# Optimization experiments

Measured on AMD Instinct MI355X. Metric: run time of the kernel, lower is better.

The kernel has to match this reference:

```python
import jax, jax.numpy as jnp
import numpy as np

INPUTS_SIZE = 128
HIDDEN_SIZE = 256
BATCH = 65536


def hard_sigmoid(x):
    # torch.nn.Hardsigmoid: relu6(x + 3) / 6
    return jnp.clip(x / 6.0 + 0.5, 0.0, 1.0)


def hard_tanh(x):
    return jnp.clip(x, -1.0, 1.0)


def setup_inputs() -> dict:
    key = jax.random.key(0)
    ks = jax.random.split(key, 8)
    cat = INPUTS_SIZE + HIDDEN_SIZE
    s = 1.0 / np.sqrt(cat)
    return {
        "inputs": jax.random.normal(ks[0], (BATCH, INPUTS_SIZE), dtype=jnp.float32),
        "h_prev": jax.random.normal(ks[1], (BATCH, HIDDEN_SIZE), dtype=jnp.float32),
        "W_z": jax.random.uniform(ks[2], (HIDDEN_SIZE, cat), jnp.float32, -s, s),
        "b_z": jax.random.uniform(ks[3], (HIDDEN_SIZE,), jnp.float32, -s, s),
        "W_r": jax.random.uniform(ks[4], (HIDDEN_SIZE, cat), jnp.float32, -s, s),
        "b_r": jax.random.uniform(ks[5], (HIDDEN_SIZE,), jnp.float32, -s, s),
        "W_h": jax.random.uniform(ks[6], (HIDDEN_SIZE, cat), jnp.float32, -s, s),
        "b_h": jax.random.uniform(ks[7], (HIDDEN_SIZE,), jnp.float32, -s, s),
    }


def reference(inputs, h_prev, W_z, b_z, W_r, b_r, W_h, b_h):
    # concat(inputs, h_prev) along feature dim: [B, I+H]
    ih = jnp.concatenate([inputs, h_prev], axis=-1)
    # update gate z and reset gate r (HardSigmoid activations)
    z = hard_sigmoid(ih @ W_z.T + b_z)  # [B, H]
    r = hard_sigmoid(ih @ W_r.T + b_r)  # [B, H]
    # candidate: concat(inputs, r * h_prev) -> linear -> HardTanh
    irh = jnp.concatenate([inputs, r * h_prev], axis=-1)
    h_tilde = hard_tanh(irh @ W_h.T + b_h)  # [B, H]
    # h_next = z * h_prev + (1 - z) * h_tilde
    h_next = z * h_prev + (1.0 - z) * h_tilde
    return h_next
```

## Files before the change

### kernel.cpp

```cpp
#include <hip/hip_runtime.h>


#define BATCH   65536
#define ISZ     128
#define HSZ     256
#define CAT     384
#define BM      64
#define NT      512
#define ROWB    768
#define ACT_B   (BM * ROWB)
#define WBUF_B  32768

using half8   = __attribute__((ext_vector_type(8))) _Float16;
using floatx4 = __attribute__((ext_vector_type(4))) float;

#define WAITV asm volatile("s_waitcnt vmcnt(0)" ::: "memory")

typedef unsigned int u32;
typedef __attribute__((address_space(1))) const u32 gu32;
typedef __attribute__((address_space(3))) u32 lu32;

__device__ __forceinline__ void gload16(const void* g, void* l) {
    __builtin_amdgcn_global_load_lds((gu32*)g, (lu32*)l, 16, 0, 0);
}

__device__ __forceinline__ float hsig(float x) {
    return fminf(fmaxf(x * (1.0f / 6.0f) + 0.5f, 0.0f), 1.0f);
}
__device__ __forceinline__ float htanh(float x) {
    return fminf(fmaxf(x, -1.0f), 1.0f);
}
__device__ __forceinline__ half8 cvt8(float4 v0, float4 v1) {
    half8 h;
    h[0] = (_Float16)v0.x; h[1] = (_Float16)v0.y;
    h[2] = (_Float16)v0.z; h[3] = (_Float16)v0.w;
    h[4] = (_Float16)v1.x; h[5] = (_Float16)v1.y;
    h[6] = (_Float16)v1.z; h[7] = (_Float16)v1.w;
    return h;
}

__global__ __launch_bounds__(256) void prep_weights(
    const float* __restrict__ Wz, const float* __restrict__ Wr,
    const float* __restrict__ Wh, _Float16* __restrict__ ws)
{
    const int m = blockIdx.y;
    const float* src = (m == 0) ? Wz : (m == 1) ? Wr : Wh;
    _Float16* dst = ws + (size_t)m * (HSZ * CAT);
    const int base = (blockIdx.x * 256 + threadIdx.x) * 8;
    float4 v0 = *(const float4*)(src + base);
    float4 v1 = *(const float4*)(src + base + 4);
    *(half8*)(dst + base) = cvt8(v0, v1);
}

__device__ __forceinline__ void issue_w(const _Float16* __restrict__ wsrc,
                                        unsigned char* wdst, int w, int lane,
                                        int kk, int nper) {
    #pragma unroll
    for (int ii = 0; ii < nper; ++ii) {
        const int i = w * nper + ii;
        const int n = i * 16 + (lane >> 2);
        const int sslot = (lane & 3) ^ ((n >> 1) & 3);
        gload16(wsrc + n * CAT + kk * 32 + sslot * 8, wdst + i * 1024);
    }
}

__device__ __forceinline__ half8 wread(const unsigned char* wbuf, int n, int lk) {
    return *(const half8*)(wbuf + n * 64 + ((lk ^ ((n >> 1) & 3)) << 4));
}

__global__ __launch_bounds__(NT, 4) void gru_kernel(
    const float* __restrict__ x, const float* __restrict__ h_prev,
    const float* __restrict__ b_z, const float* __restrict__ b_r,
    const float* __restrict__ b_h, const _Float16* __restrict__ wf,
    float* __restrict__ out)
{
    __shared__ __align__(16) unsigned char lds[ACT_B + WBUF_B];
    unsigned char* const act  = lds;
    unsigned char* const wbuf = lds + ACT_B;

    const int t    = threadIdx.x;
    const int lane = t & 63;
    const int w    = t >> 6;
    const int mg   = w >> 2;
    const int ng   = w & 3;
    const int lr   = lane & 15;
    const int lk   = lane >> 4;
    const int row0 = blockIdx.x * BM;
    const _Float16* wh = wf + 2 * HSZ * CAT;

    issue_w(wf, wbuf, w, lane, 0, 4);

    for (int c = t; c < BM * 16; c += NT) {
        int row = c >> 4, kc = c & 15;
        const float* g = x + (size_t)(row0 + row) * ISZ + kc * 8;
        float4 v0 = *(const float4*)g;
        float4 v1 = *(const float4*)(g + 4);
        *(half8*)(act + row * ROWB + ((kc * 16) ^ ((row & 7) << 4))) = cvt8(v0, v1);
    }
    for (int c = t; c < BM * 32; c += NT) {
        int row = c >> 5, kc = c & 31;
        const float* g = h_prev + (size_t)(row0 + row) * HSZ + kc * 8;
        float4 v0 = *(const float4*)g;
        float4 v1 = *(const float4*)(g + 4);
        *(half8*)(act + row * ROWB + ((256 + kc * 16) ^ ((row & 7) << 4))) = cvt8(v0, v1);
    }
    WAITV;
    __syncthreads();

    floatx4 accz[2][4] = {};
    floatx4 accr[2][4] = {};
    const int rowA = mg * 32 + lr;
    const int asw  = (rowA & 7) << 4;

    #pragma unroll 1
    for (int kk = 0; kk < 12; ++kk) {
        half8 a0 = *(const half8*)(act + rowA * ROWB        + ((kk * 64 + lk * 16) ^ asw));
        half8 a1 = *(const half8*)(act + (rowA + 16) * ROWB + ((kk * 64 + lk * 16) ^ asw));
        half8 bf[4];
        #pragma unroll
        for (int j = 0; j < 4; ++j) bf[j] = wread(wbuf, ng * 64 + j * 16 + lr, lk);
        #pragma unroll
        for (int j = 0; j < 4; ++j) {
            accz[0][j] = __builtin_amdgcn_mfma_f32_16x16x32_f16(a0, bf[j], accz[0][j], 0, 0, 0);
            accz[1][j] = __builtin_amdgcn_mfma_f32_16x16x32_f16(a1, bf[j], accz[1][j], 0, 0, 0);
        }
        #pragma unroll
        for (int j = 0; j < 4; ++j) bf[j] = wread(wbuf, 256 + ng * 64 + j * 16 + lr, lk);
        #pragma unroll
        for (int j = 0; j < 4; ++j) {
            accr[0][j] = __builtin_amdgcn_mfma_f32_16x16x32_f16(a0, bf[j], accr[0][j], 0, 0, 0);
            accr[1][j] = __builtin_amdgcn_mfma_f32_16x16x32_f16(a1, bf[j], accr[1][j], 0, 0, 0);
        }
        __syncthreads();
        if (kk < 11) {
            issue_w(wf, wbuf, w, lane, kk + 1, 4);
            WAITV;
            __syncthreads();
        }
    }

    issue_w(wh, wbuf, w, lane, 0, 2);

    float bzv[4], brv[4];
    #pragma unroll
    for (int j = 0; j < 4; ++j) {
        int col = ng * 64 + j * 16 + lr;
        bzv[j] = b_z[col];
        brv[j] = b_r[col];
    }
    #pragma unroll
    for (int f = 0; f < 2; ++f) {
        #pragma unroll
        for (int j = 0; j < 4; ++j) {
            #pragma unroll
            for (int q = 0; q < 4; ++q) {
                int row = mg * 32 + f * 16 + lk * 4 + q;
                int col = ng * 64 + j * 16 + lr;
                accz[f][j][q] = hsig(accz[f][j][q] + bzv[j]);
                float rr = hsig(accr[f][j][q] + brv[j]);
                _Float16* hp = (_Float16*)(act + row * ROWB +
                                           ((256 + col * 2) ^ ((row & 7) << 4)));
                float hv = (float)hp[0];
                hp[0] = (_Float16)(rr * hv);
            }
        }
    }
    WAITV;
    __syncthreads();

    floatx4 acch[2][4] = {};
    #pragma unroll 1
    for (int kk = 0; kk < 12; ++kk) {
        half8 a0 = *(const half8*)(act + rowA * ROWB        + ((kk * 64 + lk * 16) ^ asw));
        half8 a1 = *(const half8*)(act + (rowA + 16) * ROWB + ((kk * 64 + lk * 16) ^ asw));
        half8 bf[4];
        #pragma unroll
        for (int j = 0; j < 4; ++j) bf[j] = wread(wbuf, ng * 64 + j * 16 + lr, lk);
        #pragma unroll
        for (int j = 0; j < 4; ++j) {
            acch[0][j] = __builtin_amdgcn_mfma_f32_16x16x32_f16(a0, bf[j], acch[0][j], 0, 0, 0);
            acch[1][j] = __builtin_amdgcn_mfma_f32_16x16x32_f16(a1, bf[j], acch[1][j], 0, 0, 0);
        }
        if (kk < 11) {
            __syncthreads();
            issue_w(wh, wbuf, w, lane, kk + 1, 2);
            WAITV;
            __syncthreads();
        }
    }

    float bhv[4];
    #pragma unroll
    for (int j = 0; j < 4; ++j) bhv[j] = b_h[ng * 64 + j * 16 + lr];
    #pragma unroll
    for (int f = 0; f < 2; ++f) {
        #pragma unroll
        for (int j = 0; j < 4; ++j) {
            #pragma unroll
            for (int q = 0; q < 4; ++q) {
                int row = mg * 32 + f * 16 + lk * 4 + q;
                int col = ng * 64 + j * 16 + lr;
                float ht = htanh(acch[f][j][q] + bhv[j]);
                float zz = accz[f][j][q];
                float hv = h_prev[(size_t)(row0 + row) * HSZ + col];
                out[(size_t)(row0 + row) * HSZ + col] = zz * hv + (1.0f - zz) * ht;
            }
        }
    }
}

extern "C" void kernel_launch(void* const* d_in, const int* in_sizes, int n_in,
                              void* d_out, int out_size, void* d_ws, size_t ws_size,
                              hipStream_t stream) {
    const float* x  = (const float*)d_in[0];
    const float* h  = (const float*)d_in[1];
    const float* Wz = (const float*)d_in[2];
    const float* bz = (const float*)d_in[3];
    const float* Wr = (const float*)d_in[4];
    const float* br = (const float*)d_in[5];
    const float* Wh = (const float*)d_in[6];
    const float* bh = (const float*)d_in[7];
    _Float16* wf = (_Float16*)d_ws;

    prep_weights<<<dim3(48, 3), 256, 0, stream>>>(Wz, Wr, Wh, wf);
    gru_kernel<<<dim3(BATCH / BM), NT, 0, stream>>>(
        x, h, bz, br, bh, wf, (float*)d_out);
}
```

Measured before the change: 206.6 us.

## Double-buffer weight chunks with vmcnt-based waits to overlap loads with MFMA

Replaces the single weight buffer and its load-then-wait-all pattern with two 16 KB chunk buffers. Each chunk is fetched asynchronously while the other is consumed, and partial `s_waitcnt vmcnt(2)` waits let one chunk stay in flight; the prefetch also runs across the boundary into the candidate-gate phase. It adds `s_setprio` around MFMA bursts and folds the biases into the accumulator initial values. This is meant to hide global-to-LDS weight latency behind matrix math, at the cost of more barriers and more complex wait bookkeeping.

```diff
diff --git a/kernel.cpp b/kernel.cpp
--- a/kernel.cpp
+++ b/kernel.cpp
@@ -1,20 +1,18 @@
 #include <hip/hip_runtime.h>
 
 
-#define BATCH   65536
-#define ISZ     128
-#define HSZ     256
-#define CAT     384
-#define BM      64
-#define NT      512
-#define ROWB    768
-#define ACT_B   (BM * ROWB)
-#define WBUF_B  32768
+#define BATCH 65536
+#define ISZ   128
+#define HSZ   256
+#define CAT   384
+#define BM    64
+#define NT    512
+#define ROWB  768
+#define ACT_B (BM * ROWB)
+#define CH_B  16384
 
 using half8   = __attribute__((ext_vector_type(8))) _Float16;
 using floatx4 = __attribute__((ext_vector_type(4))) float;
-
-#define WAITV asm volatile("s_waitcnt vmcnt(0)" ::: "memory")
 
 typedef unsigned int u32;
 typedef __attribute__((address_space(1))) const u32 gu32;
@@ -23,6 +21,13 @@
 __device__ __forceinline__ void gload16(const void* g, void* l) {
     __builtin_amdgcn_global_load_lds((gu32*)g, (lu32*)l, 16, 0, 0);
 }
+
+#define BAR()      __builtin_amdgcn_s_barrier()
+#define SCHED0()   __builtin_amdgcn_sched_barrier(0)
+#define WAIT_VM2() asm volatile("s_waitcnt vmcnt(2)" ::: "memory")
+#define WAIT_VM0() asm volatile("s_waitcnt vmcnt(0)" ::: "memory")
+#define WAIT_LG0() asm volatile("s_waitcnt lgkmcnt(0)" ::: "memory")
+#define MFMA       __builtin_amdgcn_mfma_f32_16x16x32_f16
 
 __device__ __forceinline__ float hsig(float x) {
     return fminf(fmaxf(x * (1.0f / 6.0f) + 0.5f, 0.0f), 1.0f);
@@ -52,20 +57,24 @@
     *(half8*)(dst + base) = cvt8(v0, v1);
 }
 
-__device__ __forceinline__ void issue_w(const _Float16* __restrict__ wsrc,
-                                        unsigned char* wdst, int w, int lane,
-                                        int kk, int nper) {
-    #pragma unroll
-    for (int ii = 0; ii < nper; ++ii) {
-        const int i = w * nper + ii;
+__device__ __forceinline__ void issue_chunk(const _Float16* __restrict__ wf,
+                                            unsigned char* wbuf, int c,
+                                            int w, int lane) {
+    const _Float16* src = (c < 24) ? (wf + (c & 1) * (HSZ * CAT))
+                                   : (wf + 2 * (HSZ * CAT));
+    const int kk = (c < 24) ? (c >> 1) : (c - 24);
+    unsigned char* dst = wbuf + (c & 1) * CH_B;
+    #pragma unroll
+    for (int ii = 0; ii < 2; ++ii) {
+        const int i = w * 2 + ii;
         const int n = i * 16 + (lane >> 2);
-        const int sslot = (lane & 3) ^ ((n >> 1) & 3);
-        gload16(wsrc + n * CAT + kk * 32 + sslot * 8, wdst + i * 1024);
-    }
-}
-
-__device__ __forceinline__ half8 wread(const unsigned char* wbuf, int n, int lk) {
-    return *(const half8*)(wbuf + n * 64 + ((lk ^ ((n >> 1) & 3)) << 4));
+        const int ss = (lane & 3) ^ ((n >> 1) & 3);
+        gload16(src + n * CAT + kk * 32 + ss * 8, dst + i * 1024);
+    }
+}
+
+__device__ __forceinline__ half8 wread(const unsigned char* buf, int n, int lk) {
+    return *(const half8*)(buf + n * 64 + ((lk ^ ((n >> 1) & 3)) << 4));
 }
 
 __global__ __launch_bounds__(NT, 4) void gru_kernel(
@@ -74,7 +83,7 @@
     const float* __restrict__ b_h, const _Float16* __restrict__ wf,
     float* __restrict__ out)
 {
-    __shared__ __align__(16) unsigned char lds[ACT_B + WBUF_B];
+    __shared__ __align__(16) unsigned char lds[ACT_B + 2 * CH_B];
     unsigned char* const act  = lds;
     unsigned char* const wbuf = lds + ACT_B;
 
@@ -86,9 +95,23 @@
     const int lr   = lane & 15;
     const int lk   = lane >> 4;
     const int row0 = blockIdx.x * BM;
-    const _Float16* wh = wf + 2 * HSZ * CAT;
-
-    issue_w(wf, wbuf, w, lane, 0, 4);
+
+    issue_chunk(wf, wbuf, 0, w, lane);
+    issue_chunk(wf, wbuf, 1, w, lane);
+
+    float bhv[4];
+    floatx4 accz[2][4], accr[2][4];
+    #pragma unroll
+    for (int j = 0; j < 4; ++j) {
+        const int col = ng * 64 + j * 16 + lr;
+        const float vz = b_z[col];
+        const float vr = b_r[col];
+        bhv[j] = b_h[col];
+        floatx4 tz = {vz, vz, vz, vz};
+        floatx4 tr = {vr, vr, vr, vr};
+        accz[0][j] = tz; accz[1][j] = tz;
+        accr[0][j] = tr; accr[1][j] = tr;
+    }
 
     for (int c = t; c < BM * 16; c += NT) {
         int row = c >> 4, kc = c & 15;
@@ -104,60 +127,52 @@
         float4 v1 = *(const float4*)(g + 4);
         *(half8*)(act + row * ROWB + ((256 + kc * 16) ^ ((row & 7) << 4))) = cvt8(v0, v1);
     }
-    WAITV;
-    __syncthreads();
-
-    floatx4 accz[2][4] = {};
-    floatx4 accr[2][4] = {};
+    WAIT_VM0(); WAIT_LG0(); SCHED0();
+    BAR();
+
     const int rowA = mg * 32 + lr;
     const int asw  = (rowA & 7) << 4;
 
+    half8 a0, a1;
+
     #pragma unroll 1
     for (int kk = 0; kk < 12; ++kk) {
-        half8 a0 = *(const half8*)(act + rowA * ROWB        + ((kk * 64 + lk * 16) ^ asw));
-        half8 a1 = *(const half8*)(act + (rowA + 16) * ROWB + ((kk * 64 + lk * 16) ^ asw));
-        half8 bf[4];
-        #pragma unroll
-        for (int j = 0; j < 4; ++j) bf[j] = wread(wbuf, ng * 64 + j * 16 + lr, lk);
-        #pragma unroll
-        for (int j = 0; j < 4; ++j) {
-            accz[0][j] = __builtin_amdgcn_mfma_f32_16x16x32_f16(a0, bf[j], accz[0][j], 0, 0, 0);
-            accz[1][j] = __builtin_amdgcn_mfma_f32_16x16x32_f16(a1, bf[j], accz[1][j], 0, 0, 0);
-        }
-        #pragma unroll
-        for (int j = 0; j < 4; ++j) bf[j] = wread(wbuf, 256 + ng * 64 + j * 16 + lr, lk);
-        #pragma unroll
-        for (int j = 0; j < 4; ++j) {
-            accr[0][j] = __builtin_amdgcn_mfma_f32_16x16x32_f16(a0, bf[j], accr[0][j], 0, 0, 0);
-            accr[1][j] = __builtin_amdgcn_mfma_f32_16x16x32_f16(a1, bf[j], accr[1][j], 0, 0, 0);
-        }
-        __syncthreads();
-        if (kk < 11) {
-            issue_w(wf, wbuf, w, lane, kk + 1, 4);
-            WAITV;
-            __syncthreads();
-        }
-    }
-
-    issue_w(wh, wbuf, w, lane, 0, 2);
-
-    float bzv[4], brv[4];
-    #pragma unroll
-    for (int j = 0; j < 4; ++j) {
-        int col = ng * 64 + j * 16 + lr;
-        bzv[j] = b_z[col];
-        brv[j] = b_r[col];
-    }
+        WAIT_VM2(); SCHED0(); BAR();
+        a0 = *(const half8*)(act + rowA * ROWB        + ((kk * 64 + lk * 16) ^ asw));
+        a1 = *(const half8*)(act + (rowA + 16) * ROWB + ((kk * 64 + lk * 16) ^ asw));
+        __builtin_amdgcn_s_setprio(1);
+        #pragma unroll
+        for (int j = 0; j < 4; ++j) {
+            half8 bf = wread(wbuf, ng * 64 + j * 16 + lr, lk);
+            accz[0][j] = MFMA(a0, bf, accz[0][j], 0, 0, 0);
+            accz[1][j] = MFMA(a1, bf, accz[1][j], 0, 0, 0);
+        }
+        __builtin_amdgcn_s_setprio(0);
+        WAIT_LG0(); SCHED0(); BAR();
+        issue_chunk(wf, wbuf, 2 * kk + 2, w, lane);
+        WAIT_VM2(); SCHED0(); BAR();
+        __builtin_amdgcn_s_setprio(1);
+        #pragma unroll
+        for (int j = 0; j < 4; ++j) {
+            half8 bf = wread(wbuf + CH_B, ng * 64 + j * 16 + lr, lk);
+            accr[0][j] = MFMA(a0, bf, accr[0][j], 0, 0, 0);
+            accr[1][j] = MFMA(a1, bf, accr[1][j], 0, 0, 0);
+        }
+        __builtin_amdgcn_s_setprio(0);
+        WAIT_LG0(); SCHED0(); BAR();
+        issue_chunk(wf, wbuf, 2 * kk + 3, w, lane);
+    }
+
     #pragma unroll
     for (int f = 0; f < 2; ++f) {
         #pragma unroll
         for (int j = 0; j < 4; ++j) {
             #pragma unroll
             for (int q = 0; q < 4; ++q) {
-                int row = mg * 32 + f * 16 + lk * 4 + q;
-                int col = ng * 64 + j * 16 + lr;
-                accz[f][j][q] = hsig(accz[f][j][q] + bzv[j]);
-                float rr = hsig(accr[f][j][q] + brv[j]);
+                const int row = mg * 32 + f * 16 + lk * 4 + q;
+                const int col = ng * 64 + j * 16 + lr;
+                accz[f][j][q] = hsig(accz[f][j][q]);
+                float rr = hsig(accr[f][j][q]);
                 _Float16* hp = (_Float16*)(act + row * ROWB +
                                            ((256 + col * 2) ^ ((row & 7) << 4)));
                 float hv = (float)hp[0];
@@ -165,42 +180,42 @@
             }
         }
     }
-    WAITV;
-    __syncthreads();
-
-    floatx4 acch[2][4] = {};
+    WAIT_LG0();
+
+    floatx4 acch[2][4];
+    #pragma unroll
+    for (int j = 0; j < 4; ++j) {
+        floatx4 th = {bhv[j], bhv[j], bhv[j], bhv[j]};
+        acch[0][j] = th; acch[1][j] = th;
+    }
     #pragma unroll 1
     for (int kk = 0; kk < 12; ++kk) {
-        half8 a0 = *(const half8*)(act + rowA * ROWB        + ((kk * 64 + lk * 16) ^ asw));
-        half8 a1 = *(const half8*)(act + (rowA + 16) * ROWB + ((kk * 64 + lk * 16) ^ asw));
-        half8 bf[4];
-        #pragma unroll
-        for (int j = 0; j < 4; ++j) bf[j] = wread(wbuf, ng * 64 + j * 16 + lr, lk);
-        #pragma unroll
-        for (int j = 0; j < 4; ++j) {
-            acch[0][j] = __builtin_amdgcn_mfma_f32_16x16x32_f16(a0, bf[j], acch[0][j], 0, 0, 0);
-            acch[1][j] = __builtin_amdgcn_mfma_f32_16x16x32_f16(a1, bf[j], acch[1][j], 0, 0, 0);
-        }
-        if (kk < 11) {
-            __syncthreads();
-            issue_w(wh, wbuf, w, lane, kk + 1, 2);
-            WAITV;
-            __syncthreads();
-        }
-    }
-
-    float bhv[4];
-    #pragma unroll
-    for (int j = 0; j < 4; ++j) bhv[j] = b_h[ng * 64 + j * 16 + lr];
+        if (kk < 11) { WAIT_VM2(); } else { WAIT_VM0(); }
+        SCHED0(); BAR();
+        const unsigned char* buf = wbuf + (kk & 1) * CH_B;
+        a0 = *(const half8*)(act + rowA * ROWB        + ((kk * 64 + lk * 16) ^ asw));
+        a1 = *(const half8*)(act + (rowA + 16) * ROWB + ((kk * 64 + lk * 16) ^ asw));
+        __builtin_amdgcn_s_setprio(1);
+        #pragma unroll
+        for (int j = 0; j < 4; ++j) {
+            half8 bf = wread(buf, ng * 64 + j * 16 + lr, lk);
+            acch[0][j] = MFMA(a0, bf, acch[0][j], 0, 0, 0);
+            acch[1][j] = MFMA(a1, bf, acch[1][j], 0, 0, 0);
+        }
+        __builtin_amdgcn_s_setprio(0);
+        WAIT_LG0(); SCHED0(); BAR();
+        if (kk < 10) issue_chunk(wf, wbuf, 26 + kk, w, lane);
+    }
+
     #pragma unroll
     for (int f = 0; f < 2; ++f) {
         #pragma unroll
         for (int j = 0; j < 4; ++j) {
             #pragma unroll
             for (int q = 0; q < 4; ++q) {
-                int row = mg * 32 + f * 16 + lk * 4 + q;
-                int col = ng * 64 + j * 16 + lr;
-                float ht = htanh(acch[f][j][q] + bhv[j]);
+                const int row = mg * 32 + f * 16 + lk * 4 + q;
+                const int col = ng * 64 + j * 16 + lr;
+                float ht = htanh(acch[f][j][q]);
                 float zz = accz[f][j][q];
                 float hv = h_prev[(size_t)(row0 + row) * HSZ + col];
                 out[(size_t)(row0 + row) * HSZ + col] = zz * hv + (1.0f - zz) * ht;
```

Result: faster. 198.5 us (-3.9%).
